# Optimization experiments

Measured on AMD Instinct MI355X. Metric: run time of the kernel, lower is better.

## Reference

```python
import jax, jax.numpy as jnp
import numpy as np
from jax import lax

MASK_RATE = 0.2
EPS = 1e-6
H, DK = 12, 64  # heads, per-head dim


def layer_norm(x, g, b):
    mu = jnp.mean(x, axis=-1, keepdims=True)
    var = jnp.mean(jnp.square(x - mu), axis=-1, keepdims=True)
    return (x - mu) * lax.rsqrt(var + EPS) * g + b


def setup_inputs() -> dict:
    key = jax.random.key(0)
    ks = jax.random.split(key, 24)
    B, T, S, D, F, L = 64, 131072, 256, 768, 3072, 2
    w = lambda k, shp: (jax.random.normal(k, shp, jnp.float32) * 0.02)
    inp = {
        "inputs": jax.random.normal(ks[0], (B, T, 1), jnp.float32),
        "randomness": jax.random.uniform(ks[1], (B * S, 3), jnp.float32),
        "perm": jax.random.permutation(ks[2], B * S).astype(jnp.int32),
        "conv_w": w(ks[3], (512, 1, D)),
        "conv_b": jnp.zeros((D,), jnp.float32),
        "pos_emb": w(ks[4], (300, D)),
        "mask_tok": w(ks[5], (D,)),
        "agg_tok": w(ks[6], (D,)),
        "wq": w(ks[7], (L, D, D)), "bq": jnp.zeros((L, D), jnp.float32),
        "wk": w(ks[8], (L, D, D)), "bk": jnp.zeros((L, D), jnp.float32),
        "wv": w(ks[9], (L, D, D)), "bv": jnp.zeros((L, D), jnp.float32),
        "wo": w(ks[10], (L, D, D)), "bo": jnp.zeros((L, D), jnp.float32),
        "ln1_g": jnp.ones((L, D), jnp.float32), "ln1_b": jnp.zeros((L, D), jnp.float32),
        "w1": w(ks[11], (L, D, F)), "b1": jnp.zeros((L, F), jnp.float32),
        "w2": w(ks[12], (L, F, D)), "b2": jnp.zeros((L, D), jnp.float32),
        "ln2_g": jnp.ones((L, D), jnp.float32), "ln2_b": jnp.zeros((L, D), jnp.float32),
    }
    return inp


def forward(inputs, randomness, perm, conv_w, conv_b, pos_emb, mask_tok, agg_tok,
            wq, bq, wk, bk, wv, bv, wo, bo, ln1_g, ln1_b, w1, b1, w2, b2, ln2_g, ln2_b):
    # waveform -> patches: Conv1D kernel=512 stride=512 valid
    x = lax.conv_general_dilated(inputs, conv_w, window_strides=(512,), padding='VALID',
                                 dimension_numbers=('NWC', 'WIO', 'NWC')) + conv_b
    B, S, D = x.shape
    embeddings = x
    # --- BERT-style random token masking (vectorized replacement of python loop) ---
    r0, r1, r2 = randomness[:, 0], randomness[:, 1], randomness[:, 2]
    sel = r0 <= MASK_RATE
    m = (sel & (r1 <= 0.8)).astype(x.dtype).reshape(B, S)
    rnd = (sel & (r1 > 0.8) & (r2 <= 0.5)).astype(x.dtype).reshape(B, S)
    nt = (sel & (r1 > 0.8) & (r2 > 0.5)).astype(x.dtype).reshape(B, S)
    flat = lax.stop_gradient(x.reshape(B * S, D))
    shuf = flat[perm].reshape(B, S, D)
    masked = (x * (1.0 - m - rnd)[:, :, None]
              + mask_tok[None, None, :] * m[:, :, None]
              + shuf * rnd[:, :, None])
    mask_pos = m + rnd + nt
    # positional embeddings + [AGG] token
    h = masked + pos_emb[:S][None, :, :]
    h = jnp.concatenate([jnp.broadcast_to(agg_tok, (B, 1, D)), h], axis=1)  # [B, S+1, D]
    scale = 1.0 / np.sqrt(DK).astype(np.float32)
    for l in range(wq.shape[0]):
        # post-norm transformer encoder layer
        q = (jnp.einsum('bsd,de->bse', h, wq[l]) + bq[l]).reshape(B, S + 1, H, DK)
        k = (jnp.einsum('bsd,de->bse', h, wk[l]) + bk[l]).reshape(B, S + 1, H, DK)
        v = (jnp.einsum('bsd,de->bse', h, wv[l]) + bv[l]).reshape(B, S + 1, H, DK)
        scores = jnp.einsum('bqhd,bkhd->bhqk', q, k) * scale
        attn = jax.nn.softmax(scores, axis=-1)
        o = jnp.einsum('bhqk,bkhd->bqhd', attn, v).reshape(B, S + 1, D)
        o = jnp.einsum('bsd,de->bse', o, wo[l]) + bo[l]
        h = layer_norm(h + o, ln1_g[l], ln1_b[l])
        f = jax.nn.gelu(jnp.einsum('bsd,df->bsf', h, w1[l]) + b1[l])
        f = jnp.einsum('bsf,fd->bsd', f, w2[l]) + b2[l]
        h = layer_norm(h + f, ln2_g[l], ln2_b[l])
    aggregated = h[:, 0, :]
    predictions = h[:, 1:, :]  # == predictions_1d (input already [B,S,D])
    return aggregated, predictions, mask_pos, embeddings


def reference(inputs, randomness, perm, conv_w, conv_b, pos_emb, mask_tok, agg_tok,
              wq, bq, wk, bk, wv, bv, wo, bo, ln1_g, ln1_b, w1, b1, w2, b2, ln2_g, ln2_b):
    return forward(inputs, randomness, perm, conv_w, conv_b, pos_emb, mask_tok, agg_tok,
                   wq, bq, wk, bk, wv, bv, wo, bo, ln1_g, ln1_b, w1, b1, w2, b2, ln2_g, ln2_b)
```

## Files before the change

kernel.cpp:

```cpp
#include <hip/hip_runtime.h>
#include <hip/hip_bf16.h>
#include <math.h>

#define BB 64
#define SS 256
#define SP 257
#define DD 768
#define FF 3072
#define HH 12
#define DKK 64
#define ROWS (BB*SP)
#define MCONV (BB*SS)
#define RB ((size_t)ROWS * DD)

typedef short bf16x8 __attribute__((ext_vector_type(8)));
typedef float f32x4 __attribute__((ext_vector_type(4)));
typedef unsigned short ushort8v __attribute__((ext_vector_type(8)));

__device__ __forceinline__ ushort f2bf(float x) {
    union { __hip_bfloat16 h; ushort u; } c;
    c.h = __float2bfloat16(x);
    return c.u;
}
__device__ __forceinline__ float bf2f(ushort u) {
    union { __hip_bfloat16 h; ushort u; } c;
    c.u = u;
    return __bfloat162float(c.h);
}

__device__ __forceinline__ float gelu_tanh_f(float x) {
    float x3 = x * x * x;
    float u = 0.7978845608028654f * (x + 0.044715f * x3);
    return 0.5f * x * (1.0f + tanhf(u));
}

template <bool IS_MAX>
__device__ __forceinline__ float blk_reduce(float v, float* red4) {
    #pragma unroll
    for (int o = 32; o > 0; o >>= 1) {
        float other = __shfl_down(v, o, 64);
        v = IS_MAX ? fmaxf(v, other) : (v + other);
    }
    __syncthreads();
    if ((threadIdx.x & 63) == 0) red4[threadIdx.x >> 6] = v;
    __syncthreads();
    if (IS_MAX) return fmaxf(fmaxf(red4[0], red4[1]), fmaxf(red4[2], red4[3]));
    return red4[0] + red4[1] + red4[2] + red4[3];
}

__global__ __launch_bounds__(256) void wt_kernel(
    const float* __restrict__ W, ushort* __restrict__ Wt, int K, int N)
{
    __shared__ float tile[32][33];
    const int k0 = blockIdx.x * 32, n0 = blockIdx.y * 32;
    const int t = threadIdx.x;
    {
        const int r = t >> 3, c4 = (t & 7) * 4;
        float4 v = *reinterpret_cast<const float4*>(&W[(size_t)(k0 + r) * N + n0 + c4]);
        tile[r][c4 + 0] = v.x; tile[r][c4 + 1] = v.y;
        tile[r][c4 + 2] = v.z; tile[r][c4 + 3] = v.w;
    }
    __syncthreads();
    {
        const int n = t >> 3, k4 = (t & 7) * 4;
        ushort4 o;
        o.x = f2bf(tile[k4 + 0][n]); o.y = f2bf(tile[k4 + 1][n]);
        o.z = f2bf(tile[k4 + 2][n]); o.w = f2bf(tile[k4 + 3][n]);
        *reinterpret_cast<ushort4*>(&Wt[(size_t)(n0 + n) * K + k0 + k4]) = o;
    }
}

template <bool A_F32, bool C_BF16, bool GELU>
__global__ __launch_bounds__(256) void mfma_gemm(
    const void* __restrict__ Ap, const ushort* __restrict__ Bt,
    const float* __restrict__ bias, void* __restrict__ Cp,
    int M, int N, int K)
{
    __shared__ ushort As[64][72];
    __shared__ ushort Bs[128][72];
    const int tid = threadIdx.x;
    const int lane = tid & 63, wave = tid >> 6;
    const int wr = wave & 1, wc = wave >> 1;
    const int row0 = blockIdx.y * 64, col0 = blockIdx.x * 128;

    f32x4 acc[2][4];
    #pragma unroll
    for (int m = 0; m < 2; ++m)
        #pragma unroll
        for (int n = 0; n < 4; ++n)
            acc[m][n] = (f32x4){0.f, 0.f, 0.f, 0.f};

    const int arow = tid >> 2, akq = (tid & 3) * 16;
    const int brow = tid >> 1, bkh = (tid & 1) * 32;

    for (int k0 = 0; k0 < K; k0 += 64) {
        if (A_F32) {
            const float* A = (const float*)Ap;
            const float* src = &A[(size_t)(row0 + arow) * K + k0 + akq];
            float4 v0 = *reinterpret_cast<const float4*>(src + 0);
            float4 v1 = *reinterpret_cast<const float4*>(src + 4);
            float4 v2 = *reinterpret_cast<const float4*>(src + 8);
            float4 v3 = *reinterpret_cast<const float4*>(src + 12);
            ushort8v u0, u1;
            u0[0]=f2bf(v0.x); u0[1]=f2bf(v0.y); u0[2]=f2bf(v0.z); u0[3]=f2bf(v0.w);
            u0[4]=f2bf(v1.x); u0[5]=f2bf(v1.y); u0[6]=f2bf(v1.z); u0[7]=f2bf(v1.w);
            u1[0]=f2bf(v2.x); u1[1]=f2bf(v2.y); u1[2]=f2bf(v2.z); u1[3]=f2bf(v2.w);
            u1[4]=f2bf(v3.x); u1[5]=f2bf(v3.y); u1[6]=f2bf(v3.z); u1[7]=f2bf(v3.w);
            *reinterpret_cast<ushort8v*>(&As[arow][akq]) = u0;
            *reinterpret_cast<ushort8v*>(&As[arow][akq + 8]) = u1;
        } else {
            const ushort* A = (const ushort*)Ap;
            const ushort* src = &A[(size_t)(row0 + arow) * K + k0 + akq];
            *reinterpret_cast<ushort8v*>(&As[arow][akq]) =
                *reinterpret_cast<const ushort8v*>(src);
            *reinterpret_cast<ushort8v*>(&As[arow][akq + 8]) =
                *reinterpret_cast<const ushort8v*>(src + 8);
        }
        {
            const ushort* src = &Bt[(size_t)(col0 + brow) * K + k0 + bkh];
            #pragma unroll
            for (int j = 0; j < 4; ++j)
                *reinterpret_cast<ushort8v*>(&Bs[brow][bkh + 8 * j]) =
                    *reinterpret_cast<const ushort8v*>(src + 8 * j);
        }
        __syncthreads();
        #pragma unroll
        for (int ks = 0; ks < 2; ++ks) {
            bf16x8 af[2], bfr[4];
            #pragma unroll
            for (int m = 0; m < 2; ++m)
                af[m] = *reinterpret_cast<const bf16x8*>(
                    &As[wr * 32 + m * 16 + (lane & 15)][ks * 32 + (lane >> 4) * 8]);
            #pragma unroll
            for (int n = 0; n < 4; ++n)
                bfr[n] = *reinterpret_cast<const bf16x8*>(
                    &Bs[wc * 64 + n * 16 + (lane & 15)][ks * 32 + (lane >> 4) * 8]);
            #pragma unroll
            for (int m = 0; m < 2; ++m)
                #pragma unroll
                for (int n = 0; n < 4; ++n)
                    acc[m][n] = __builtin_amdgcn_mfma_f32_16x16x32_bf16(
                        af[m], bfr[n], acc[m][n], 0, 0, 0);
        }
        __syncthreads();
    }

    #pragma unroll
    for (int m = 0; m < 2; ++m) {
        #pragma unroll
        for (int n = 0; n < 4; ++n) {
            const int col = col0 + wc * 64 + n * 16 + (lane & 15);
            const float bcol = bias[col];
            #pragma unroll
            for (int j = 0; j < 4; ++j) {
                const int row = row0 + wr * 32 + m * 16 + (lane >> 4) * 4 + j;
                float v = acc[m][n][j] + bcol;
                if (GELU) v = gelu_tanh_f(v);
                if (C_BF16) ((ushort*)Cp)[(size_t)row * N + col] = f2bf(v);
                else        ((float*)Cp)[(size_t)row * N + col] = v;
            }
        }
    }
}

__global__ __launch_bounds__(256) void build_h_kernel(
    const float* __restrict__ emb, const float* __restrict__ rnd3,
    const int* __restrict__ perm, const float* __restrict__ pos_emb,
    const float* __restrict__ mask_tok, const float* __restrict__ agg_tok,
    float* __restrict__ h, float* __restrict__ mask_pos)
{
    const int sf = blockIdx.x;
    const int b = blockIdx.y;
    const int t = threadIdx.x;
    float* hrow = h + ((size_t)b * SP + sf) * DD;
    if (sf == 0) {
        #pragma unroll
        for (int i = 0; i < 3; ++i) hrow[t + 256 * i] = agg_tok[t + 256 * i];
        return;
    }
    const int s = sf - 1;
    const int idx = b * SS + s;
    const float r0 = rnd3[idx * 3 + 0];
    const float r1 = rnd3[idx * 3 + 1];
    const float r2 = rnd3[idx * 3 + 2];
    const bool sel = (r0 <= 0.2f);
    const float m  = (sel && r1 <= 0.8f) ? 1.f : 0.f;
    const float rn = (sel && r1 > 0.8f && r2 <= 0.5f) ? 1.f : 0.f;
    const float nt = (sel && r1 > 0.8f && r2 > 0.5f) ? 1.f : 0.f;
    if (t == 0) mask_pos[idx] = m + rn + nt;
    const int p = perm[idx];
    const float* xrow = emb + (size_t)idx * DD;
    const float* srow = emb + (size_t)p * DD;
    const float keep = 1.f - m - rn;
    #pragma unroll
    for (int i = 0; i < 3; ++i) {
        const int c = t + 256 * i;
        hrow[c] = xrow[c] * keep + mask_tok[c] * m + srow[c] * rn + pos_emb[s * DD + c];
    }
}

__global__ __launch_bounds__(256) void vt_kernel(
    const ushort* __restrict__ V, ushort* __restrict__ Vt)
{
    const int bh = blockIdx.x;
    const int b = bh / HH, h = bh % HH;
    const int t = threadIdx.x;
    __shared__ ushort tile[64][65];
    const size_t vtb = (size_t)bh * 64 * 288;
    const int d = t & 63, kk = t >> 6;
    const int kq = t & 63, dg = t >> 6;
    for (int kt = 0; kt < 5; ++kt) {
        #pragma unroll
        for (int i = 0; i < 16; ++i) {
            const int r = kk + 4 * i;
            const int kg = kt * 64 + r;
            tile[r][d] = (kg < SP) ? V[((size_t)b * SP + kg) * DD + h * 64 + d] : (ushort)0;
        }
        __syncthreads();
        #pragma unroll
        for (int i = 0; i < 16; ++i) {
            const int dd2 = dg + 4 * i;
            const int k = kt * 64 + kq;
            if (k < 288) Vt[vtb + (size_t)dd2 * 288 + k] = tile[kq][dd2];
        }
        __syncthreads();
    }
}

__global__ __launch_bounds__(256) void attn_mfma(
    const ushort* __restrict__ Q, const ushort* __restrict__ K,
    const ushort* __restrict__ Vt, ushort* __restrict__ O)
{
    const int h = blockIdx.x, b = blockIdx.y;
    const int t = threadIdx.x, lane = t & 63, w = t >> 6;
    const int lg = lane >> 4, lr = lane & 15;
    __shared__ ushort Pl[4][16][296];

    const size_t qkbase = ((size_t)b * SP) * DD + (size_t)h * DKK;
    const size_t vtbase = (size_t)(b * HH + h) * 64 * 288;

    #pragma unroll
    for (int i = 0; i < 4; ++i) Pl[w][lr][272 + lg * 4 + i] = 0;

    for (int p = 0; p < 5; ++p) {
        const int q0 = p * 64 + w * 16;
        const int qr = min(q0 + lr, SP - 1);
        bf16x8 aq0 = *reinterpret_cast<const bf16x8*>(&Q[qkbase + (size_t)qr * DD + lg * 8]);
        bf16x8 aq1 = *reinterpret_cast<const bf16x8*>(&Q[qkbase + (size_t)qr * DD + 32 + lg * 8]);

        f32x4 sc[17];
        #pragma unroll
        for (int n = 0; n < 17; ++n) {
            const int kr = min(n * 16 + lr, SP - 1);
            const ushort* kp = &K[qkbase + (size_t)kr * DD + lg * 8];
            bf16x8 bk0 = *reinterpret_cast<const bf16x8*>(kp);
            bf16x8 bk1 = *reinterpret_cast<const bf16x8*>(kp + 32);
            f32x4 a = (f32x4){0.f, 0.f, 0.f, 0.f};
            a = __builtin_amdgcn_mfma_f32_16x16x32_bf16(aq0, bk0, a, 0, 0, 0);
            a = __builtin_amdgcn_mfma_f32_16x16x32_bf16(aq1, bk1, a, 0, 0, 0);
            sc[n] = a;
        }

        float rmax[4] = {-1e30f, -1e30f, -1e30f, -1e30f};
        #pragma unroll
        for (int n = 0; n < 17; ++n) {
            const int kcol = n * 16 + lr;
            if (kcol >= SP) {
                sc[n] = (f32x4){-1e30f, -1e30f, -1e30f, -1e30f};
            } else {
                sc[n] *= 0.125f;
            }
            #pragma unroll
            for (int j = 0; j < 4; ++j) rmax[j] = fmaxf(rmax[j], sc[n][j]);
        }
        #pragma unroll
        for (int msk = 1; msk <= 8; msk <<= 1)
            #pragma unroll
            for (int j = 0; j < 4; ++j)
                rmax[j] = fmaxf(rmax[j], __shfl_xor(rmax[j], msk, 64));

        float rsum[4] = {0.f, 0.f, 0.f, 0.f};
        #pragma unroll
        for (int n = 0; n < 17; ++n) {
            #pragma unroll
            for (int j = 0; j < 4; ++j) {
                const float e = __expf(sc[n][j] - rmax[j]);
                rsum[j] += e;
                Pl[w][lg * 4 + j][n * 16 + lr] = f2bf(e);
            }
        }
        #pragma unroll
        for (int msk = 1; msk <= 8; msk <<= 1)
            #pragma unroll
            for (int j = 0; j < 4; ++j)
                rsum[j] += __shfl_xor(rsum[j], msk, 64);

        __syncthreads();

        f32x4 o[4];
        #pragma unroll
        for (int dn = 0; dn < 4; ++dn) o[dn] = (f32x4){0.f, 0.f, 0.f, 0.f};
        #pragma unroll
        for (int kb = 0; kb < 9; ++kb) {
            bf16x8 pa = *reinterpret_cast<const bf16x8*>(&Pl[w][lr][kb * 32 + lg * 8]);
            #pragma unroll
            for (int dn = 0; dn < 4; ++dn) {
                bf16x8 bv = *reinterpret_cast<const bf16x8*>(
                    &Vt[vtbase + (size_t)(dn * 16 + lr) * 288 + kb * 32 + lg * 8]);
                o[dn] = __builtin_amdgcn_mfma_f32_16x16x32_bf16(pa, bv, o[dn], 0, 0, 0);
            }
        }

        float rinv[4];
        #pragma unroll
        for (int j = 0; j < 4; ++j) rinv[j] = 1.f / rsum[j];
        #pragma unroll
        for (int dn = 0; dn < 4; ++dn) {
            #pragma unroll
            for (int j = 0; j < 4; ++j) {
                const int q = q0 + lg * 4 + j;
                if (q < SP)
                    O[qkbase + (size_t)q * DD + dn * 16 + lr] = f2bf(o[dn][j] * rinv[j]);
            }
        }
        __syncthreads();
    }
}

__global__ __launch_bounds__(256) void add_ln_kernel(
    float* __restrict__ h, const ushort* __restrict__ r,
    const float* __restrict__ g, const float* __restrict__ bta)
{
    const int row = blockIdx.x;
    const int t = threadIdx.x;
    __shared__ float red4[4];
    float* hp = h + (size_t)row * DD;
    const ushort* rp = r + (size_t)row * DD;
    const float x0 = hp[t]       + bf2f(rp[t]);
    const float x1 = hp[t + 256] + bf2f(rp[t + 256]);
    const float x2 = hp[t + 512] + bf2f(rp[t + 512]);
    const float s = blk_reduce<false>(x0 + x1 + x2, red4);
    const float mu = s * (1.f / 768.f);
    const float d0 = x0 - mu, d1 = x1 - mu, d2 = x2 - mu;
    const float v = blk_reduce<false>(d0 * d0 + d1 * d1 + d2 * d2, red4);
    const float inv = rsqrtf(v * (1.f / 768.f) + 1e-6f);
    hp[t]       = d0 * inv * g[t]       + bta[t];
    hp[t + 256] = d1 * inv * g[t + 256] + bta[t + 256];
    hp[t + 512] = d2 * inv * g[t + 512] + bta[t + 512];
}

__global__ __launch_bounds__(256) void out_copy_kernel(
    const float* __restrict__ h, float* __restrict__ agg, float* __restrict__ pred)
{
    const int sf = blockIdx.x;
    const int b = blockIdx.y;
    const int t = threadIdx.x;
    const float* hp = h + ((size_t)b * SP + sf) * DD;
    if (sf == 0) {
        #pragma unroll
        for (int i = 0; i < 3; ++i) agg[(size_t)b * DD + t + 256 * i] = hp[t + 256 * i];
    } else {
        float* pp = pred + ((size_t)(b * SS + sf - 1)) * DD;
        #pragma unroll
        for (int i = 0; i < 3; ++i) pp[t + 256 * i] = hp[t + 256 * i];
    }
}

extern "C" void kernel_launch(void* const* d_in, const int* in_sizes, int n_in,
                              void* d_out, int out_size, void* d_ws, size_t ws_size,
                              hipStream_t stream)
{
    const float* inputs   = (const float*)d_in[0];
    const float* rnd3     = (const float*)d_in[1];
    const int*   perm     = (const int*)d_in[2];
    const float* conv_w   = (const float*)d_in[3];
    const float* conv_b   = (const float*)d_in[4];
    const float* pos_emb  = (const float*)d_in[5];
    const float* mask_tok = (const float*)d_in[6];
    const float* agg_tok  = (const float*)d_in[7];
    const float* wq = (const float*)d_in[8];
    const float* bq = (const float*)d_in[9];
    const float* wk = (const float*)d_in[10];
    const float* bk = (const float*)d_in[11];
    const float* wv = (const float*)d_in[12];
    const float* bv = (const float*)d_in[13];
    const float* wo = (const float*)d_in[14];
    const float* bo = (const float*)d_in[15];
    const float* ln1_g = (const float*)d_in[16];
    const float* ln1_b = (const float*)d_in[17];
    const float* w1 = (const float*)d_in[18];
    const float* b1 = (const float*)d_in[19];
    const float* w2 = (const float*)d_in[20];
    const float* b2 = (const float*)d_in[21];
    const float* ln2_g = (const float*)d_in[22];
    const float* ln2_b = (const float*)d_in[23];

    float* out = (float*)d_out;
    float* agg_out  = out;
    float* pred_out = out + 49152;
    float* mask_out = out + 49152 + 12582912;
    float* emb_out  = out + 49152 + 12582912 + 16384;

    char* base = (char*)d_ws;
    float*  h    = (float*)base;
    ushort* qb   = (ushort*)(base + RB * 4);
    ushort* kb   = qb + RB;
    ushort* vb   = kb + RB;
    ushort* ob   = vb + RB;
    ushort* mid  = qb;
    ushort* vt   = ob + RB;
    ushort* rbuf = vt;
    ushort* wptr = vt + (size_t)768 * 64 * 288;

    ushort* convT = wptr;                          wptr += (size_t)DD * 512;
    ushort* wqT[2]; ushort* wkT[2]; ushort* wvT[2]; ushort* woT[2];
    ushort* w1T[2]; ushort* w2T[2];
    for (int l = 0; l < 2; ++l) {
        wqT[l] = wptr; wptr += (size_t)DD * DD;
        wkT[l] = wptr; wptr += (size_t)DD * DD;
        wvT[l] = wptr; wptr += (size_t)DD * DD;
        woT[l] = wptr; wptr += (size_t)DD * DD;
        w1T[l] = wptr; wptr += (size_t)DD * FF;
        w2T[l] = wptr; wptr += (size_t)FF * DD;
    }

    const dim3 blk(256);

    wt_kernel<<<dim3(512 / 32, DD / 32), blk, 0, stream>>>(conv_w, convT, 512, DD);
    for (int l = 0; l < 2; ++l) {
        wt_kernel<<<dim3(DD / 32, DD / 32), blk, 0, stream>>>(wq + (size_t)l*DD*DD, wqT[l], DD, DD);
        wt_kernel<<<dim3(DD / 32, DD / 32), blk, 0, stream>>>(wk + (size_t)l*DD*DD, wkT[l], DD, DD);
        wt_kernel<<<dim3(DD / 32, DD / 32), blk, 0, stream>>>(wv + (size_t)l*DD*DD, wvT[l], DD, DD);
        wt_kernel<<<dim3(DD / 32, DD / 32), blk, 0, stream>>>(wo + (size_t)l*DD*DD, woT[l], DD, DD);
        wt_kernel<<<dim3(DD / 32, FF / 32), blk, 0, stream>>>(w1 + (size_t)l*DD*FF, w1T[l], DD, FF);
        wt_kernel<<<dim3(FF / 32, DD / 32), blk, 0, stream>>>(w2 + (size_t)l*FF*DD, w2T[l], FF, DD);
    }

    mfma_gemm<true, false, false><<<dim3(DD / 128, MCONV / 64), blk, 0, stream>>>(
        inputs, convT, conv_b, emb_out, MCONV, DD, 512);

    build_h_kernel<<<dim3(SP, BB), blk, 0, stream>>>(
        emb_out, rnd3, perm, pos_emb, mask_tok, agg_tok, h, mask_out);

    for (int l = 0; l < 2; ++l) {
        mfma_gemm<true, true, false><<<dim3(DD / 128, ROWS / 64), blk, 0, stream>>>(
            h, wqT[l], bq + l * DD, qb, ROWS, DD, DD);
        mfma_gemm<true, true, false><<<dim3(DD / 128, ROWS / 64), blk, 0, stream>>>(
            h, wkT[l], bk + l * DD, kb, ROWS, DD, DD);
        mfma_gemm<true, true, false><<<dim3(DD / 128, ROWS / 64), blk, 0, stream>>>(
            h, wvT[l], bv + l * DD, vb, ROWS, DD, DD);

        vt_kernel<<<dim3(BB * HH), blk, 0, stream>>>(vb, vt);
        attn_mfma<<<dim3(HH, BB), blk, 0, stream>>>(qb, kb, vt, ob);

        mfma_gemm<false, true, false><<<dim3(DD / 128, ROWS / 64), blk, 0, stream>>>(
            ob, woT[l], bo + l * DD, rbuf, ROWS, DD, DD);

        add_ln_kernel<<<dim3(ROWS), blk, 0, stream>>>(h, rbuf, ln1_g + l * DD, ln1_b + l * DD);

        mfma_gemm<true, true, true><<<dim3(FF / 128, ROWS / 64), blk, 0, stream>>>(
            h, w1T[l], b1 + l * FF, mid, ROWS, FF, DD);
        mfma_gemm<false, true, false><<<dim3(DD / 128, ROWS / 64), blk, 0, stream>>>(
            mid, w2T[l], b2 + l * DD, rbuf, ROWS, DD, FF);

        add_ln_kernel<<<dim3(ROWS), blk, 0, stream>>>(h, rbuf, ln2_g + l * DD, ln2_b + l * DD);
    }

    out_copy_kernel<<<dim3(SP, BB), blk, 0, stream>>>(h, agg_out, pred_out);
}
```

Measured before the change: 1.642 ms.

## Use 128x128 GEMM tiles with direct global-to-LDS loads and bf16 activation copies

Replaces the 64x128 GEMM with a 128x128 tile that loads A and B straight into LDS through global_load_lds, which removes the register staging and the padded LDS layout. The fp32 activations that were converted inside every GEMM are now written once as a bf16 copy by build_h and add_ln (stored in the prediction output buffer as scratch), and the conv input gets its own conversion kernel. M is padded to 16512 so it divides into 128-row tiles, and the scratch buffers are enlarged to match. The risks are LDS bank conflicts in the unpadded layout, padded rows reading garbage, and an extra bf16 write pass.

```diff
diff --git a/kernel.cpp b/kernel.cpp
--- a/kernel.cpp
+++ b/kernel.cpp
@@ -10,8 +10,10 @@
 #define HH 12
 #define DKK 64
 #define ROWS (BB*SP)
+#define MPAD 16512
 #define MCONV (BB*SS)
 #define RB ((size_t)ROWS * DD)
+#define PRB ((size_t)MPAD * DD)
 
 typedef short bf16x8 __attribute__((ext_vector_type(8)));
 typedef float f32x4 __attribute__((ext_vector_type(4)));
@@ -32,6 +34,12 @@
     float x3 = x * x * x;
     float u = 0.7978845608028654f * (x + 0.044715f * x3);
     return 0.5f * x * (1.0f + tanhf(u));
+}
+
+__device__ __forceinline__ void gload16(const ushort* g, ushort* l) {
+    __builtin_amdgcn_global_load_lds(
+        (__attribute__((address_space(1))) void*)(g),
+        (__attribute__((address_space(3))) void*)(l), 16, 0, 0);
 }
 
 template <bool IS_MAX>
@@ -46,6 +54,16 @@
     __syncthreads();
     if (IS_MAX) return fmaxf(fmaxf(red4[0], red4[1]), fmaxf(red4[2], red4[3]));
     return red4[0] + red4[1] + red4[2] + red4[3];
+}
+
+__global__ __launch_bounds__(256) void conv_in_bf_kernel(
+    const float* __restrict__ in, ushort* __restrict__ out)
+{
+    const size_t i = ((size_t)blockIdx.x * 256 + threadIdx.x) * 4;
+    float4 v = *reinterpret_cast<const float4*>(&in[i]);
+    ushort4 o;
+    o.x = f2bf(v.x); o.y = f2bf(v.y); o.z = f2bf(v.z); o.w = f2bf(v.w);
+    *reinterpret_cast<ushort4*>(&out[i]) = o;
 }
 
 __global__ __launch_bounds__(256) void wt_kernel(
@@ -70,90 +88,71 @@
     }
 }
 
-template <bool A_F32, bool C_BF16, bool GELU>
-__global__ __launch_bounds__(256) void mfma_gemm(
-    const void* __restrict__ Ap, const ushort* __restrict__ Bt,
+template <bool C_BF16, bool GELU>
+__global__ __launch_bounds__(256) void gemm128(
+    const ushort* __restrict__ A, const ushort* __restrict__ Bt,
     const float* __restrict__ bias, void* __restrict__ Cp,
     int M, int N, int K)
 {
-    __shared__ ushort As[64][72];
-    __shared__ ushort Bs[128][72];
+    __shared__ ushort As[128 * 64];
+    __shared__ ushort Bs[128 * 64];
     const int tid = threadIdx.x;
-    const int lane = tid & 63, wave = tid >> 6;
-    const int wr = wave & 1, wc = wave >> 1;
-    const int row0 = blockIdx.y * 64, col0 = blockIdx.x * 128;
-
-    f32x4 acc[2][4];
+    const int lane = tid & 63, w = tid >> 6;
+    const int wr = w & 1, wc = w >> 1;
+    const int lg = lane >> 4, lr = lane & 15;
+    const int row0 = blockIdx.y * 128, col0 = blockIdx.x * 128;
+
+    f32x4 acc[4][4];
     #pragma unroll
-    for (int m = 0; m < 2; ++m)
+    for (int m = 0; m < 4; ++m)
         #pragma unroll
         for (int n = 0; n < 4; ++n)
             acc[m][n] = (f32x4){0.f, 0.f, 0.f, 0.f};
 
-    const int arow = tid >> 2, akq = (tid & 3) * 16;
-    const int brow = tid >> 1, bkh = (tid & 1) * 32;
+    const int g_rowoff = w * 8 + (lane >> 3);
+    const int g_colu   = (lane & 7) * 8;
 
     for (int k0 = 0; k0 < K; k0 += 64) {
-        if (A_F32) {
-            const float* A = (const float*)Ap;
-            const float* src = &A[(size_t)(row0 + arow) * K + k0 + akq];
-            float4 v0 = *reinterpret_cast<const float4*>(src + 0);
-            float4 v1 = *reinterpret_cast<const float4*>(src + 4);
-            float4 v2 = *reinterpret_cast<const float4*>(src + 8);
-            float4 v3 = *reinterpret_cast<const float4*>(src + 12);
-            ushort8v u0, u1;
-            u0[0]=f2bf(v0.x); u0[1]=f2bf(v0.y); u0[2]=f2bf(v0.z); u0[3]=f2bf(v0.w);
-            u0[4]=f2bf(v1.x); u0[5]=f2bf(v1.y); u0[6]=f2bf(v1.z); u0[7]=f2bf(v1.w);
-            u1[0]=f2bf(v2.x); u1[1]=f2bf(v2.y); u1[2]=f2bf(v2.z); u1[3]=f2bf(v2.w);
-            u1[4]=f2bf(v3.x); u1[5]=f2bf(v3.y); u1[6]=f2bf(v3.z); u1[7]=f2bf(v3.w);
-            *reinterpret_cast<ushort8v*>(&As[arow][akq]) = u0;
-            *reinterpret_cast<ushort8v*>(&As[arow][akq + 8]) = u1;
-        } else {
-            const ushort* A = (const ushort*)Ap;
-            const ushort* src = &A[(size_t)(row0 + arow) * K + k0 + akq];
-            *reinterpret_cast<ushort8v*>(&As[arow][akq]) =
-                *reinterpret_cast<const ushort8v*>(src);
-            *reinterpret_cast<ushort8v*>(&As[arow][akq + 8]) =
-                *reinterpret_cast<const ushort8v*>(src + 8);
-        }
-        {
-            const ushort* src = &Bt[(size_t)(col0 + brow) * K + k0 + bkh];
-            #pragma unroll
-            for (int j = 0; j < 4; ++j)
-                *reinterpret_cast<ushort8v*>(&Bs[brow][bkh + 8 * j]) =
-                    *reinterpret_cast<const ushort8v*>(src + 8 * j);
-        }
-        __syncthreads();
+        #pragma unroll
+        for (int r = 0; r < 4; ++r) {
+            const int row = r * 32 + g_rowoff;
+            gload16(&A[(size_t)(row0 + row) * K + k0 + g_colu],
+                    &As[r * 2048 + w * 512]);
+            gload16(&Bt[(size_t)(col0 + row) * K + k0 + g_colu],
+                    &Bs[r * 2048 + w * 512]);
+        }
+        __syncthreads();
+
         #pragma unroll
         for (int ks = 0; ks < 2; ++ks) {
-            bf16x8 af[2], bfr[4];
-            #pragma unroll
-            for (int m = 0; m < 2; ++m)
+            bf16x8 af[4], bf[4];
+            #pragma unroll
+            for (int m = 0; m < 4; ++m)
                 af[m] = *reinterpret_cast<const bf16x8*>(
-                    &As[wr * 32 + m * 16 + (lane & 15)][ks * 32 + (lane >> 4) * 8]);
+                    &As[(wr * 64 + m * 16 + lr) * 64 + ks * 32 + lg * 8]);
             #pragma unroll
             for (int n = 0; n < 4; ++n)
-                bfr[n] = *reinterpret_cast<const bf16x8*>(
-                    &Bs[wc * 64 + n * 16 + (lane & 15)][ks * 32 + (lane >> 4) * 8]);
-            #pragma unroll
-            for (int m = 0; m < 2; ++m)
+                bf[n] = *reinterpret_cast<const bf16x8*>(
+                    &Bs[(wc * 64 + n * 16 + lr) * 64 + ks * 32 + lg * 8]);
+            #pragma unroll
+            for (int m = 0; m < 4; ++m)
                 #pragma unroll
                 for (int n = 0; n < 4; ++n)
                     acc[m][n] = __builtin_amdgcn_mfma_f32_16x16x32_bf16(
-                        af[m], bfr[n], acc[m][n], 0, 0, 0);
+                        af[m], bf[n], acc[m][n], 0, 0, 0);
         }
         __syncthreads();
     }
 
     #pragma unroll
-    for (int m = 0; m < 2; ++m) {
+    for (int m = 0; m < 4; ++m) {
         #pragma unroll
         for (int n = 0; n < 4; ++n) {
-            const int col = col0 + wc * 64 + n * 16 + (lane & 15);
+            const int col = col0 + wc * 64 + n * 16 + lr;
             const float bcol = bias[col];
             #pragma unroll
             for (int j = 0; j < 4; ++j) {
-                const int row = row0 + wr * 32 + m * 16 + (lane >> 4) * 4 + j;
+                const int row = row0 + wr * 64 + m * 16 + lg * 4 + j;
                 float v = acc[m][n][j] + bcol;
                 if (GELU) v = gelu_tanh_f(v);
                 if (C_BF16) ((ushort*)Cp)[(size_t)row * N + col] = f2bf(v);
@@ -167,15 +166,21 @@
     const float* __restrict__ emb, const float* __restrict__ rnd3,
     const int* __restrict__ perm, const float* __restrict__ pos_emb,
     const float* __restrict__ mask_tok, const float* __restrict__ agg_tok,
-    float* __restrict__ h, float* __restrict__ mask_pos)
+    float* __restrict__ h, ushort* __restrict__ hb, float* __restrict__ mask_pos)
 {
     const int sf = blockIdx.x;
     const int b = blockIdx.y;
     const int t = threadIdx.x;
-    float* hrow = h + ((size_t)b * SP + sf) * DD;
+    const size_t ro = ((size_t)b * SP + sf) * DD;
+    float* hrow = h + ro;
+    ushort* hbrow = hb + ro;
     if (sf == 0) {
         #pragma unroll
-        for (int i = 0; i < 3; ++i) hrow[t + 256 * i] = agg_tok[t + 256 * i];
+        for (int i = 0; i < 3; ++i) {
+            const float v = agg_tok[t + 256 * i];
+            hrow[t + 256 * i] = v;
+            hbrow[t + 256 * i] = f2bf(v);
+        }
         return;
     }
     const int s = sf - 1;
@@ -195,7 +200,9 @@
     #pragma unroll
     for (int i = 0; i < 3; ++i) {
         const int c = t + 256 * i;
-        hrow[c] = xrow[c] * keep + mask_tok[c] * m + srow[c] * rn + pos_emb[s * DD + c];
+        const float v = xrow[c] * keep + mask_tok[c] * m + srow[c] * rn + pos_emb[s * DD + c];
+        hrow[c] = v;
+        hbrow[c] = f2bf(v);
     }
 }
 
@@ -328,13 +335,14 @@
 }
 
 __global__ __launch_bounds__(256) void add_ln_kernel(
-    float* __restrict__ h, const ushort* __restrict__ r,
+    float* __restrict__ h, ushort* __restrict__ hb, const ushort* __restrict__ r,
     const float* __restrict__ g, const float* __restrict__ bta)
 {
     const int row = blockIdx.x;
     const int t = threadIdx.x;
     __shared__ float red4[4];
     float* hp = h + (size_t)row * DD;
+    ushort* hbp = hb + (size_t)row * DD;
     const ushort* rp = r + (size_t)row * DD;
     const float x0 = hp[t]       + bf2f(rp[t]);
     const float x1 = hp[t + 256] + bf2f(rp[t + 256]);
@@ -344,9 +352,12 @@
     const float d0 = x0 - mu, d1 = x1 - mu, d2 = x2 - mu;
     const float v = blk_reduce<false>(d0 * d0 + d1 * d1 + d2 * d2, red4);
     const float inv = rsqrtf(v * (1.f / 768.f) + 1e-6f);
-    hp[t]       = d0 * inv * g[t]       + bta[t];
-    hp[t + 256] = d1 * inv * g[t + 256] + bta[t + 256];
-    hp[t + 512] = d2 * inv * g[t + 512] + bta[t + 512];
+    const float y0 = d0 * inv * g[t]       + bta[t];
+    const float y1 = d1 * inv * g[t + 256] + bta[t + 256];
+    const float y2 = d2 * inv * g[t + 512] + bta[t + 512];
+    hp[t]       = y0;  hbp[t]       = f2bf(y0);
+    hp[t + 256] = y1;  hbp[t + 256] = f2bf(y1);
+    hp[t + 512] = y2;  hbp[t + 512] = f2bf(y2);
 }
 
 __global__ __launch_bounds__(256) void out_copy_kernel(
@@ -401,14 +412,17 @@
     float* mask_out = out + 49152 + 12582912;
     float* emb_out  = out + 49152 + 12582912 + 16384;
 
+    ushort* hb = (ushort*)pred_out;
+
     char* base = (char*)d_ws;
     float*  h    = (float*)base;
     ushort* qb   = (ushort*)(base + RB * 4);
-    ushort* kb   = qb + RB;
-    ushort* vb   = kb + RB;
-    ushort* ob   = vb + RB;
+    ushort* kb   = qb + PRB;
+    ushort* vb   = kb + PRB;
+    ushort* ob   = vb + PRB;
     ushort* mid  = qb;
-    ushort* vt   = ob + RB;
+    ushort* inbf = qb;
+    ushort* vt   = ob + PRB;
     ushort* rbuf = vt;
     ushort* wptr = vt + (size_t)768 * 64 * 288;
 
@@ -426,6 +440,7 @@
 
     const dim3 blk(256);
 
+    conv_in_bf_kernel<<<dim3((MCONV * 512) / 1024), blk, 0, stream>>>(inputs, inbf);
     wt_kernel<<<dim3(512 / 32, DD / 32), blk, 0, stream>>>(conv_w, convT, 512, DD);
     for (int l = 0; l < 2; ++l) {
         wt_kernel<<<dim3(DD / 32, DD / 32), blk, 0, stream>>>(wq + (size_t)l*DD*DD, wqT[l], DD, DD);
@@ -436,34 +451,36 @@
         wt_kernel<<<dim3(FF / 32, DD / 32), blk, 0, stream>>>(w2 + (size_t)l*FF*DD, w2T[l], FF, DD);
     }
 
-    mfma_gemm<true, false, false><<<dim3(DD / 128, MCONV / 64), blk, 0, stream>>>(
-        inputs, convT, conv_b, emb_out, MCONV, DD, 512);
+    gemm128<false, false><<<dim3(DD / 128, MCONV / 128), blk, 0, stream>>>(
+        inbf, convT, conv_b, emb_out, MCONV, DD, 512);
 
     build_h_kernel<<<dim3(SP, BB), blk, 0, stream>>>(
-        emb_out, rnd3, perm, pos_emb, mask_tok, agg_tok, h, mask_out);
+        emb_out, rnd3, perm, pos_emb, mask_tok, agg_tok, h, hb, mask_out);
 
     for (int l = 0; l < 2; ++l) {
-        mfma_gemm<true, true, false><<<dim3(DD / 128, ROWS / 64), blk, 0, stream>>>(
-            h, wqT[l], bq + l * DD, qb, ROWS, DD, DD);
-        mfma_gemm<true, true, false><<<dim3(DD / 128, ROWS / 64), blk, 0, stream>>>(
-            h, wkT[l], bk + l * DD, kb, ROWS, DD, DD);
-        mfma_gemm<true, true, false><<<dim3(DD / 128, ROWS / 64), blk, 0, stream>>>(
-            h, wvT[l], bv + l * DD, vb, ROWS, DD, DD);
+        gemm128<true, false><<<dim3(DD / 128, MPAD / 128), blk, 0, stream>>>(
+            hb, wqT[l], bq + l * DD, qb, MPAD, DD, DD);
+        gemm128<true, false><<<dim3(DD / 128, MPAD / 128), blk, 0, stream>>>(
+            hb, wkT[l], bk + l * DD, kb, MPAD, DD, DD);
+        gemm128<true, false><<<dim3(DD / 128, MPAD / 128), blk, 0, stream>>>(
+            hb, wvT[l], bv + l * DD, vb, MPAD, DD, DD);
 
         vt_kernel<<<dim3(BB * HH), blk, 0, stream>>>(vb, vt);
         attn_mfma<<<dim3(HH, BB), blk, 0, stream>>>(qb, kb, vt, ob);
 
-        mfma_gemm<false, true, false><<<dim3(DD / 128, ROWS / 64), blk, 0, stream>>>(
-            ob, woT[l], bo + l * DD, rbuf, ROWS, DD, DD);
-
-        add_ln_kernel<<<dim3(ROWS), blk, 0, stream>>>(h, rbuf, ln1_g + l * DD, ln1_b + l * DD);
-
-        mfma_gemm<true, true, true><<<dim3(FF / 128, ROWS / 64), blk, 0, stream>>>(
-            h, w1T[l], b1 + l * FF, mid, ROWS, FF, DD);
-        mfma_gemm<false, true, false><<<dim3(DD / 128, ROWS / 64), blk, 0, stream>>>(
-            mid, w2T[l], b2 + l * DD, rbuf, ROWS, DD, FF);
-
-        add_ln_kernel<<<dim3(ROWS), blk, 0, stream>>>(h, rbuf, ln2_g + l * DD, ln2_b + l * DD);
+        gemm128<true, false><<<dim3(DD / 128, MPAD / 128), blk, 0, stream>>>(
+            ob, woT[l], bo + l * DD, rbuf, MPAD, DD, DD);
+
+        add_ln_kernel<<<dim3(ROWS), blk, 0, stream>>>(
+            h, hb, rbuf, ln1_g + l * DD, ln1_b + l * DD);
+
+        gemm128<true, true><<<dim3(FF / 128, MPAD / 128), blk, 0, stream>>>(
+            hb, w1T[l], b1 + l * FF, mid, MPAD, FF, DD);
+        gemm128<true, false><<<dim3(DD / 128, MPAD / 128), blk, 0, stream>>>(
+            mid, w2T[l], b2 + l * DD, rbuf, MPAD, DD, FF);
+
+        add_ln_kernel<<<dim3(ROWS), blk, 0, stream>>>(
+            h, hb, rbuf, ln2_g + l * DD, ln2_b + l * DD);
     }
 
     out_copy_kernel<<<dim3(SP, BB), blk, 0, stream>>>(h, agg_out, pred_out);
```

Measured after the change: 1.599 ms. 2.6% less time.
